# Kernel tuning notes

Measured on AMD Instinct MI355X. Metric: run time of the kernel, lower is better.

## Reference

```python
import jax, jax.numpy as jnp
import numpy as np

LANES = 4
EPS = 1e-8

def _rms_norm(z):
    # utils.rms: RMS-normalize along last dim
    return z * jax.lax.rsqrt(jnp.mean(z * z, axis=-1, keepdims=True) + EPS)

def _combine(left, right, W):
    # one scan combine step: tiny SDPA over the 4 lanes per token
    B, T, C = left.shape
    hd = C // LANES
    q = left.reshape(B, T, LANES, hd)
    k = right.reshape(B, T, LANES, hd)
    # ProcrustesButterflyLinear: orthogonal mixing of the two operands
    v = ((left + right) @ W).reshape(B, T, LANES, hd)
    scores = jnp.einsum('btld,btmd->btlm', q, k) * (hd ** -0.5)  # [B,T,4,4]
    att = jax.nn.softmax(scores, axis=-1)
    z = jnp.einsum('btlm,btmd->btld', att, v)
    denom = (1.0 + jnp.arange(LANES, dtype=z.dtype))[None, None, :, None]
    z = _rms_norm(z) / denom
    return left + z.reshape(B, T, C)

def _pscan2(x, W, identity):
    # parallel inclusive scan (Hillis-Steele, log2(T) combine steps)
    B, T, C = x.shape
    d = 1
    while d < T:
        ident = jnp.broadcast_to(identity.astype(x.dtype), (B, d, C))
        shifted = jnp.concatenate([ident, x[:, :-d]], axis=1)
        x = _combine(shifted, x, W)
        d *= 2
    return x

def setup_inputs() -> dict:
    key = jax.random.key(0)
    ks = jax.random.split(key, 6)
    B, T, C = 4, 2048, 1024
    s = 0.02
    x = jax.random.normal(ks[0], (B, T, C), dtype=jnp.float32)
    W_up = jax.random.normal(ks[1], (C, C), dtype=jnp.float32) * s
    W_v = jax.random.normal(ks[2], (C, C), dtype=jnp.float32) * s
    W_proj = jax.random.normal(ks[3], (C, C), dtype=jnp.float32) * s
    identity = jax.random.uniform(ks[4], (C,), dtype=jnp.float32)
    W_scan_raw = jax.random.normal(ks[5], (C, C), dtype=jnp.float32) * s
    return {"x": x, "W_up": W_up, "W_v": W_v, "W_proj": W_proj,
            "identity": identity, "W_scan_raw": W_scan_raw}

def reference(x, W_up, W_v, W_proj, identity, W_scan_raw):
    # Procrustes orthogonalization of the scanner weight (nearest orthogonal matrix)
    U, _, Vt = jnp.linalg.svd(W_scan_raw, full_matrices=False)
    W = U @ Vt
    q = x @ W_up.T      # self.up(x)
    v = x @ W_v.T       # self.v_attn(x)
    q = _pscan2(q, W, identity)
    Y = (q * v) @ W_proj.T   # c_proj; dropout = identity at eval
    return (Y, q)
```

## Files before the change

### kernel.cpp

```cpp
#include <hip/hip_runtime.h>
#include <hip/hip_bf16.h>

#define DEVINL __device__ __forceinline__

constexpr int B_   = 4;
constexpr int T_   = 2048;
constexpr int C_   = 1024;
constexpr int NTOK = B_ * T_;
constexpr int HD   = 256;

typedef unsigned short u16;
typedef __attribute__((ext_vector_type(8))) short  frag_ab;
typedef __attribute__((ext_vector_type(4))) float  frag_cd;
typedef __attribute__((ext_vector_type(8))) u16    u16x8;
typedef __attribute__((ext_vector_type(4))) u16    u16x4;

DEVINL float bf2f(u16 u) {
    unsigned int x = ((unsigned int)u) << 16;
    return __uint_as_float(x);
}
DEVINL u16 f2bf(float f) {
    unsigned int x = __float_as_uint(f);
    unsigned int r = (x + 0x7fffu + ((x >> 16) & 1u)) >> 16;
    return (u16)r;
}
DEVINL void split2(float f, u16& h, u16& l) {
    h = f2bf(f);
    l = f2bf(f - bf2f(h));
}
DEVINL float wave_reduce(float v) {
    #pragma unroll
    for (int off = 32; off > 0; off >>= 1) v += __shfl_down(v, off, 64);
    return v;
}
DEVINL void gl_lds16(const void* g, void* l) {
    __builtin_amdgcn_global_load_lds(
        (const __attribute__((address_space(1))) unsigned int*)g,
        (__attribute__((address_space(3))) unsigned int*)l, 16, 0, 0);
}

DEVINL void swizzle_block(int& bx, int& by) {
    const int hw = (int)(blockIdx.x + gridDim.x * blockIdx.y);
    if (gridDim.x == 8 && gridDim.y == 64) {
        const int xcd = hw & 7, idx = hw >> 3;
        by = xcd * 8 + (idx & 7);
        bx = idx >> 3;
    } else { bx = blockIdx.x; by = blockIdx.y; }
}

__global__ __launch_bounds__(256) void detect_k(const u16* __restrict__ w,
                                                int* __restrict__ flag)
{
    int tid = threadIdx.x;
    int cnt = 0;
    for (int i = tid; i < 4096; i += 256) {
        u16 u = w[2 * i];
        int e = (u >> 7) & 0xFF;
        if (u == 0 || (e >= 96 && e <= 134)) cnt++;
    }
    __shared__ int sh[256];
    sh[tid] = cnt; __syncthreads();
    for (int s = 128; s > 0; s >>= 1) {
        if (tid < s) sh[tid] += sh[tid + s];
        __syncthreads();
    }
    if (tid == 0) *flag = (sh[0] > 2048) ? 1 : 0;
}

__global__ __launch_bounds__(256) void conv_k(const void* __restrict__ src,
                                              float* __restrict__ dst, int n,
                                              const int* __restrict__ flag)
{
    int i = blockIdx.x * 256 + threadIdx.x;
    if (i >= n) return;
    if (*flag) dst[i] = bf2f(((const u16*)src)[i]);
    else       dst[i] = ((const float*)src)[i];
}

__global__ __launch_bounds__(256) void conv_split_k(const void* __restrict__ src,
                                                    u16* __restrict__ H,
                                                    u16* __restrict__ L, int n4,
                                                    const int* __restrict__ flag)
{
    int i = blockIdx.x * 256 + threadIdx.x;
    if (i >= n4) return;
    float f[4];
    if (*flag) {
        u16x4 u = ((const u16x4*)src)[i];
        f[0] = bf2f(u[0]); f[1] = bf2f(u[1]); f[2] = bf2f(u[2]); f[3] = bf2f(u[3]);
    } else {
        float4 v = ((const float4*)src)[i];
        f[0] = v.x; f[1] = v.y; f[2] = v.z; f[3] = v.w;
    }
    u16x4 h, lo;
    #pragma unroll
    for (int r = 0; r < 4; ++r) { u16 a, b; split2(f[r], a, b); h[r] = a; lo[r] = b; }
    ((u16x4*)H)[i] = h; ((u16x4*)L)[i] = lo;
}

__global__ __launch_bounds__(256) void convb_k(const void* __restrict__ src,
                                               u16* __restrict__ out, int n4,
                                               const int* __restrict__ flag)
{
    int i = blockIdx.x * 256 + threadIdx.x;
    if (i >= n4) return;
    u16x4 o;
    if (*flag) {
        o = ((const u16x4*)src)[i];
    } else {
        float4 v = ((const float4*)src)[i];
        o[0] = f2bf(v.x); o[1] = f2bf(v.y); o[2] = f2bf(v.z); o[3] = f2bf(v.w);
    }
    ((u16x4*)out)[i] = o;
}

__global__ __launch_bounds__(256) void sumsq_k(const float* __restrict__ X,
                                               float* __restrict__ sumsq)
{
    int i = blockIdx.x * 256 + threadIdx.x;
    float f = X[i];
    float p = wave_reduce(f * f);
    __shared__ float r[4];
    int lane = threadIdx.x & 63, w = threadIdx.x >> 6;
    if (lane == 0) r[w] = p;
    __syncthreads();
    if (threadIdx.x == 0) atomicAdd(sumsq, r[0] + r[1] + r[2] + r[3]);
}

__global__ __launch_bounds__(256) void scale_k(float* __restrict__ X,
                                               const float* __restrict__ sumsq)
{
    int i = blockIdx.x * 256 + threadIdx.x;
    float F = sqrtf(*sumsq);
    float s = 16.0f / (1.1f * F);
    X[i] *= s;
}

__global__ __launch_bounds__(256) void split_k(const float* __restrict__ X,
                                               u16* __restrict__ H,
                                               u16* __restrict__ L, int n)
{
    int i = blockIdx.x * 256 + threadIdx.x;
    if (i >= n) return;
    u16 hi, lo; split2(X[i], hi, lo);
    H[i] = hi; L[i] = lo;
}

__global__ __launch_bounds__(256) void transpose_split_k(
    const float* __restrict__ W, u16* __restrict__ Th, u16* __restrict__ Tl)
{
    __shared__ float tile[32][33];
    const int k0 = blockIdx.y * 32;
    const int n0 = blockIdx.x * 32;
    const int tx = threadIdx.x & 31, ty = threadIdx.x >> 5;
    #pragma unroll
    for (int r = 0; r < 32; r += 8)
        tile[ty + r][tx] = W[(size_t)(k0 + ty + r) * C_ + n0 + tx];
    __syncthreads();
    #pragma unroll
    for (int r = 0; r < 32; r += 8) {
        float f = tile[tx][ty + r];
        size_t idx = (size_t)(n0 + ty + r) * C_ + k0 + tx;
        u16 hi, lo; split2(f, hi, lo);
        Th[idx] = hi; Tl[idx] = lo;
    }
}

__global__ __launch_bounds__(256) void gemm_split64(
    const u16* __restrict__ Ah, const u16* __restrict__ Al,
    const u16* __restrict__ Bh, const u16* __restrict__ Bl,
    float* __restrict__ Cf, u16* __restrict__ Ch, u16* __restrict__ Cl,
    const float* __restrict__ D, float alpha, float beta,
    int M, int N, int K,
    u16* __restrict__ Th, u16* __restrict__ Tl)
{
    __shared__ u16 sAh[2][4][64][32];
    __shared__ u16 sAl[2][4][64][32];
    __shared__ u16 sBh[2][4][64][32];
    __shared__ u16 sBl[2][4][64][32];

    const int bm = blockIdx.y * 64, bn = blockIdx.x * 64;
    const int tid = threadIdx.x;
    const int l = tid & 63, w = tid >> 6;
    const int mbase = (w & 1) * 32, nbase = (w >> 1) * 32;
    const int lrow = l & 15, kq = (l >> 4) << 3;

    frag_cd acc[2][2];
    #pragma unroll
    for (int i = 0; i < 2; ++i)
        #pragma unroll
        for (int j = 0; j < 2; ++j)
            #pragma unroll
            for (int r = 0; r < 4; ++r) acc[i][j][r] = 0.0f;

    auto STAGE = [&](int buf, int k0) {
        #pragma unroll
        for (int half = 0; half < 4; ++half) {
            const int c   = tid + half * 256;
            const int ks  = c >> 8;
            const int row = (c >> 2) & 63;
            const int ko  = ks * 32 + (c & 3) * 8;
            const size_t ga = (size_t)(bm + row) * K + k0 + ko;
            const size_t gb = (size_t)(bn + row) * K + k0 + ko;
            gl_lds16(Ah + ga, &sAh[0][0][0][0] + buf * 8192 + (c << 3));
            gl_lds16(Al + ga, &sAl[0][0][0][0] + buf * 8192 + (c << 3));
            gl_lds16(Bh + gb, &sBh[0][0][0][0] + buf * 8192 + (c << 3));
            gl_lds16(Bl + gb, &sBl[0][0][0][0] + buf * 8192 + (c << 3));
        }
    };

    STAGE(0, 0);
    __syncthreads();
    const int NT = K >> 7;
    int cur = 0;
    for (int t = 0; t < NT; ++t) {
        if (t + 1 < NT) STAGE(cur ^ 1, (t + 1) << 7);
        #pragma unroll
        for (int ks = 0; ks < 4; ++ks) {
            frag_ab ah[2], al2[2], bh[2], bl2[2];
            #pragma unroll
            for (int i = 0; i < 2; ++i) {
                const int ro = mbase + 16 * i + lrow;
                ah[i]  = *(const frag_ab*)&sAh[cur][ks][ro][kq];
                al2[i] = *(const frag_ab*)&sAl[cur][ks][ro][kq];
            }
            #pragma unroll
            for (int j = 0; j < 2; ++j) {
                const int ro = nbase + 16 * j + lrow;
                bh[j]  = *(const frag_ab*)&sBh[cur][ks][ro][kq];
                bl2[j] = *(const frag_ab*)&sBl[cur][ks][ro][kq];
            }
            #pragma unroll
            for (int i = 0; i < 2; ++i)
                #pragma unroll
                for (int j = 0; j < 2; ++j) {
                    acc[i][j] = __builtin_amdgcn_mfma_f32_16x16x32_bf16(
                        ah[i], bh[j], acc[i][j], 0, 0, 0);
                    acc[i][j] = __builtin_amdgcn_mfma_f32_16x16x32_bf16(
                        al2[i], bh[j], acc[i][j], 0, 0, 0);
                    acc[i][j] = __builtin_amdgcn_mfma_f32_16x16x32_bf16(
                        ah[i], bl2[j], acc[i][j], 0, 0, 0);
                    acc[i][j] = __builtin_amdgcn_mfma_f32_16x16x32_bf16(
                        al2[i], bl2[j], acc[i][j], 0, 0, 0);
                }
        }
        __syncthreads();
        cur ^= 1;
    }

    const int quad = l >> 4;
    u16* tileH = &sAh[0][0][0][0];
    u16* tileL = &sAl[0][0][0][0];
    #pragma unroll
    for (int i = 0; i < 2; ++i) {
        #pragma unroll
        for (int j = 0; j < 2; ++j) {
            const int coln = bn + nbase + 16 * j + lrow;
            #pragma unroll
            for (int r = 0; r < 4; ++r) {
                const int rowm = bm + mbase + 16 * i + quad * 4 + r;
                const size_t idx = (size_t)rowm * N + coln;
                float v = beta * acc[i][j][r];
                if (D) v += alpha * D[idx];
                if (Cf) Cf[idx] = v;
                u16 hi, lo; split2(v, hi, lo);
                if (Ch) { Ch[idx] = hi; Cl[idx] = lo; }
                if (Th) {
                    const int rl = mbase + 16 * i + quad * 4 + r;
                    const int cl = nbase + 16 * j + lrow;
                    tileH[rl * 68 + cl] = hi;
                    tileL[rl * 68 + cl] = lo;
                }
            }
        }
    }
    if (Th) {
        __syncthreads();
        const int jj  = tid >> 2;
        const int ii0 = (tid & 3) << 4;
        u16x8 ph0, ph1, pl0, pl1;
        #pragma unroll
        for (int e = 0; e < 8; ++e) {
            ph0[e] = tileH[(ii0 + e) * 68 + jj];
            pl0[e] = tileL[(ii0 + e) * 68 + jj];
            ph1[e] = tileH[(ii0 + 8 + e) * 68 + jj];
            pl1[e] = tileL[(ii0 + 8 + e) * 68 + jj];
        }
        const size_t tb = (size_t)(bn + jj) * N + bm + ii0;
        *(u16x8*)&Th[tb]     = ph0;
        *(u16x8*)&Th[tb + 8] = ph1;
        *(u16x8*)&Tl[tb]     = pl0;
        *(u16x8*)&Tl[tb + 8] = pl1;
    }
}

__global__ __launch_bounds__(256) void gemm_split(
    const u16* __restrict__ Ah, const u16* __restrict__ Al,
    const u16* __restrict__ Bh, const u16* __restrict__ Bl,
    float* __restrict__ Cf, u16* __restrict__ Ch, u16* __restrict__ Cl,
    int M, int N, int K)
{
    __shared__ u16 sAh[2][128][32];
    __shared__ u16 sAl[2][128][32];
    __shared__ u16 sBh[2][128][32];
    __shared__ u16 sBl[2][128][32];

    int bx, by; swizzle_block(bx, by);
    const int bm = by * 128, bn = bx * 128;
    const int tid = threadIdx.x;
    const int l = tid & 63, w = tid >> 6;
    const int mbase = (w & 1) * 64, nbase = (w >> 1) * 64;
    const int lrow = l & 15, kq = (l >> 4) << 3;

    frag_cd acc[4][4];
    #pragma unroll
    for (int i = 0; i < 4; ++i)
        #pragma unroll
        for (int j = 0; j < 4; ++j)
            #pragma unroll
            for (int r = 0; r < 4; ++r) acc[i][j][r] = 0.0f;

    auto STAGE = [&](int buf, int k0) {
        #pragma unroll
        for (int half = 0; half < 2; ++half) {
            const int c   = tid + half * 256;
            const int row = c >> 2;
            const int ko  = (c & 3) << 3;
            const size_t ga = (size_t)(bm + row) * K + k0 + ko;
            const size_t gb = (size_t)(bn + row) * K + k0 + ko;
            gl_lds16(Ah + ga, &sAh[buf][0][0] + (c << 3));
            gl_lds16(Al + ga, &sAl[buf][0][0] + (c << 3));
            gl_lds16(Bh + gb, &sBh[buf][0][0] + (c << 3));
            gl_lds16(Bl + gb, &sBl[buf][0][0] + (c << 3));
        }
    };

    STAGE(0, 0);
    __syncthreads();
    const int NT = K >> 5;
    int cur = 0;
    for (int t = 0; t < NT; ++t) {
        if (t + 1 < NT) STAGE(cur ^ 1, (t + 1) << 5);
        frag_ab ah[4], al4[4], bh[4], bl4[4];
        #pragma unroll
        for (int i = 0; i < 4; ++i) {
            const int ro = mbase + 16 * i + lrow;
            ah[i]  = *(const frag_ab*)&sAh[cur][ro][kq];
            al4[i] = *(const frag_ab*)&sAl[cur][ro][kq];
        }
        #pragma unroll
        for (int j = 0; j < 4; ++j) {
            const int ro = nbase + 16 * j + lrow;
            bh[j]  = *(const frag_ab*)&sBh[cur][ro][kq];
            bl4[j] = *(const frag_ab*)&sBl[cur][ro][kq];
        }
        #pragma unroll
        for (int i = 0; i < 4; ++i)
            #pragma unroll
            for (int j = 0; j < 4; ++j) {
                acc[i][j] = __builtin_amdgcn_mfma_f32_16x16x32_bf16(
                    ah[i], bh[j], acc[i][j], 0, 0, 0);
                acc[i][j] = __builtin_amdgcn_mfma_f32_16x16x32_bf16(
                    al4[i], bh[j], acc[i][j], 0, 0, 0);
                acc[i][j] = __builtin_amdgcn_mfma_f32_16x16x32_bf16(
                    ah[i], bl4[j], acc[i][j], 0, 0, 0);
            }
        __syncthreads();
        cur ^= 1;
    }

    const int quad = l >> 4;
    #pragma unroll
    for (int i = 0; i < 4; ++i) {
        #pragma unroll
        for (int j = 0; j < 4; ++j) {
            const int coln = bn + nbase + 16 * j + lrow;
            #pragma unroll
            for (int r = 0; r < 4; ++r) {
                const int rowm = bm + mbase + 16 * i + quad * 4 + r;
                const size_t idx = (size_t)rowm * N + coln;
                float v = acc[i][j][r];
                if (Cf) Cf[idx] = v;
                if (Ch) { u16 hi, lo; split2(v, hi, lo); Ch[idx] = hi; Cl[idx] = lo; }
            }
        }
    }
}

__global__ __launch_bounds__(256) void gemm_bf16(
    const u16* __restrict__ Ab, const u16* __restrict__ Bb,
    void* __restrict__ Cdst, int cmode, const int* __restrict__ flag,
    int M, int N, int K)
{
    __shared__ u16 As[2][2][128][32];
    __shared__ u16 Bs[2][2][128][32];
    const int cbf = (cmode == 1) ? *flag : 0;

    int bx, by; swizzle_block(bx, by);
    const int bm = by * 128, bn = bx * 128;
    const int tid = threadIdx.x;
    const int l = tid & 63, w = tid >> 6;
    const int mbase = (w & 1) * 64, nbase = (w >> 1) * 64;
    const int lrow = l & 15, kq = (l >> 4) << 3;

    frag_cd acc[4][4];
    #pragma unroll
    for (int i = 0; i < 4; ++i)
        #pragma unroll
        for (int j = 0; j < 4; ++j)
            #pragma unroll
            for (int r = 0; r < 4; ++r) acc[i][j][r] = 0.0f;

    auto STAGE = [&](int buf, int k0) {
        #pragma unroll
        for (int half = 0; half < 4; ++half) {
            const int c   = tid + half * 256;
            const int ks  = c >> 9;
            const int row = (c >> 2) & 127;
            const int ko  = ks * 32 + (c & 3) * 8;
            const size_t ga = (size_t)(bm + row) * K + k0 + ko;
            const size_t gb = (size_t)(bn + row) * K + k0 + ko;
            gl_lds16(Ab + ga, &As[buf][0][0][0] + (c << 3));
            gl_lds16(Bb + gb, &Bs[buf][0][0][0] + (c << 3));
        }
    };

    STAGE(0, 0);
    __syncthreads();
    const int NT = K >> 6;
    int cur = 0;
    for (int t = 0; t < NT; ++t) {
        if (t + 1 < NT) STAGE(cur ^ 1, (t + 1) << 6);
        #pragma unroll
        for (int ks = 0; ks < 2; ++ks) {
            frag_ab a[4], b[4];
            #pragma unroll
            for (int i = 0; i < 4; ++i)
                a[i] = *(const frag_ab*)&As[cur][ks][mbase + 16 * i + lrow][kq];
            #pragma unroll
            for (int j = 0; j < 4; ++j)
                b[j] = *(const frag_ab*)&Bs[cur][ks][nbase + 16 * j + lrow][kq];
            #pragma unroll
            for (int i = 0; i < 4; ++i)
                #pragma unroll
                for (int j = 0; j < 4; ++j)
                    acc[i][j] = __builtin_amdgcn_mfma_f32_16x16x32_bf16(
                        a[i], b[j], acc[i][j], 0, 0, 0);
        }
        __syncthreads();
        cur ^= 1;
    }

    const int quad = l >> 4;
    #pragma unroll
    for (int i = 0; i < 4; ++i) {
        #pragma unroll
        for (int j = 0; j < 4; ++j) {
            const int coln = bn + nbase + 16 * j + lrow;
            #pragma unroll
            for (int r = 0; r < 4; ++r) {
                const int rowm = bm + mbase + 16 * i + quad * 4 + r;
                const size_t idx = (size_t)rowm * N + coln;
                float v = acc[i][j][r];
                if (cbf) ((u16*)Cdst)[idx] = f2bf(v);
                else     ((float*)Cdst)[idx] = v;
            }
        }
    }
}

__global__ __launch_bounds__(256) void qvb_k(const u16* __restrict__ qh,
                                             const u16* __restrict__ ql,
                                             const float* __restrict__ V,
                                             u16* __restrict__ out, int n4)
{
    int i = blockIdx.x * 256 + threadIdx.x;
    if (i >= n4) return;
    u16x4 h = ((const u16x4*)qh)[i], lo = ((const u16x4*)ql)[i];
    float4 v = ((const float4*)V)[i];
    u16x4 o;
    o[0] = f2bf((bf2f(h[0]) + bf2f(lo[0])) * v.x);
    o[1] = f2bf((bf2f(h[1]) + bf2f(lo[1])) * v.y);
    o[2] = f2bf((bf2f(h[2]) + bf2f(lo[2])) * v.z);
    o[3] = f2bf((bf2f(h[3]) + bf2f(lo[3])) * v.w);
    ((u16x4*)out)[i] = o;
}

__global__ __launch_bounds__(256) void store_split_k(
    const u16* __restrict__ h, const u16* __restrict__ l,
    void* __restrict__ out, int n4, size_t off4,
    const int* __restrict__ flag)
{
    int i = blockIdx.x * 256 + threadIdx.x;
    if (i >= n4) return;
    u16x4 hh = ((const u16x4*)h)[i], ll = ((const u16x4*)l)[i];
    float4 f;
    f.x = bf2f(hh[0]) + bf2f(ll[0]);
    f.y = bf2f(hh[1]) + bf2f(ll[1]);
    f.z = bf2f(hh[2]) + bf2f(ll[2]);
    f.w = bf2f(hh[3]) + bf2f(ll[3]);
    if (*flag) {
        u16x4 o; o[0] = f2bf(f.x); o[1] = f2bf(f.y); o[2] = f2bf(f.z); o[3] = f2bf(f.w);
        ((u16x4*)out)[off4 + i] = o;
    } else {
        ((float4*)out)[off4 + i] = f;
    }
}

__global__ __launch_bounds__(256) void idw2_k(
    const float* __restrict__ identf, const float* __restrict__ W,
    float* __restrict__ idW)
{
    const int b = blockIdx.x;
    const int j = threadIdx.x;
    float a0 = 0, a1 = 0, a2 = 0, a3 = 0;
    #pragma unroll
    for (int ii = 0; ii < 16; ++ii) {
        const int i = b * 16 + ii;
        const float s = identf[i];
        const float* row = W + (size_t)i * C_;
        a0 += s * row[j];
        a1 += s * row[j + 256];
        a2 += s * row[j + 512];
        a3 += s * row[j + 768];
    }
    atomicAdd(idW + j, a0);       atomicAdd(idW + j + 256, a1);
    atomicAdd(idW + j + 512, a2); atomicAdd(idW + j + 768, a3);
}

__global__ __launch_bounds__(256) void combine3_k(
    const u16* __restrict__ curh, const u16* __restrict__ curl,
    const float* __restrict__ xW,
    const float* __restrict__ idW, const float* __restrict__ identf,
    u16* __restrict__ nxth, u16* __restrict__ nxtl, int d)
{
    const int token = blockIdx.x;
    const int t = token & (T_ - 1);
    const int tid = threadIdx.x;
    const bool hl = (t >= d);
    const size_t rbase = (size_t)token * C_;
    const size_t lbase = hl ? (size_t)(token - d) * C_ : 0;
    const float* leftW  = hl ? xW + lbase : idW;
    const float* rightW = xW + rbase;

    const int e0   = tid << 2;
    const int a    = tid >> 6;
    const int dd   = (tid & 63) << 2;
    const int lane = tid & 63;

    float q4[4], k4[4], v4[4];
    {
        u16x4 kh = *(const u16x4*)&curh[rbase + e0];
        u16x4 kl = *(const u16x4*)&curl[rbase + e0];
        #pragma unroll
        for (int e = 0; e < 4; ++e) k4[e] = bf2f(kh[e]) + bf2f(kl[e]);
        if (hl) {
            u16x4 qh = *(const u16x4*)&curh[lbase + e0];
            u16x4 ql = *(const u16x4*)&curl[lbase + e0];
            #pragma unroll
            for (int e = 0; e < 4; ++e) q4[e] = bf2f(qh[e]) + bf2f(ql[e]);
        } else {
            float4 iv = *(const float4*)&identf[e0];
            q4[0] = iv.x; q4[1] = iv.y; q4[2] = iv.z; q4[3] = iv.w;
        }
        float4 lw = *(const float4*)&leftW[e0];
        float4 rw = *(const float4*)&rightW[e0];
        v4[0] = lw.x + rw.x; v4[1] = lw.y + rw.y;
        v4[2] = lw.z + rw.z; v4[3] = lw.w + rw.w;
    }

    __shared__ float ks[4][256];
    __shared__ float vs[4][256];
    __shared__ float red[16];
    __shared__ float att[16];
    __shared__ float rs4[4];
    {
        float4 kv = { k4[0], k4[1], k4[2], k4[3] };
        float4 vv = { v4[0], v4[1], v4[2], v4[3] };
        *(float4*)&ks[a][dd] = kv;
        *(float4*)&vs[a][dd] = vv;
    }
    __syncthreads();

    #pragma unroll
    for (int b = 0; b < 4; ++b) {
        float4 kk = *(const float4*)&ks[b][dd];
        float pp = q4[0] * kk.x + q4[1] * kk.y + q4[2] * kk.z + q4[3] * kk.w;
        float sb = wave_reduce(pp);
        if (lane == 0) red[a * 4 + b] = sb * 0.0625f;
    }
    __syncthreads();
    if (tid < 4) {
        float s0 = red[tid * 4 + 0], s1 = red[tid * 4 + 1];
        float s2 = red[tid * 4 + 2], s3 = red[tid * 4 + 3];
        float mx = fmaxf(fmaxf(s0, s1), fmaxf(s2, s3));
        float x0 = __expf(s0 - mx), x1 = __expf(s1 - mx);
        float x2 = __expf(s2 - mx), x3 = __expf(s3 - mx);
        float inv = 1.0f / (x0 + x1 + x2 + x3);
        att[tid * 4 + 0] = x0 * inv; att[tid * 4 + 1] = x1 * inv;
        att[tid * 4 + 2] = x2 * inv; att[tid * 4 + 3] = x3 * inv;
    }
    __syncthreads();

    const float a0 = att[a * 4 + 0], a1 = att[a * 4 + 1];
    const float a2 = att[a * 4 + 2], a3 = att[a * 4 + 3];
    float4 v0 = *(const float4*)&vs[0][dd];
    float4 v1 = *(const float4*)&vs[1][dd];
    float4 v2 = *(const float4*)&vs[2][dd];
    float4 v3 = *(const float4*)&vs[3][dd];
    float z4[4];
    z4[0] = a0 * v0.x + a1 * v1.x + a2 * v2.x + a3 * v3.x;
    z4[1] = a0 * v0.y + a1 * v1.y + a2 * v2.y + a3 * v3.y;
    z4[2] = a0 * v0.z + a1 * v1.z + a2 * v2.z + a3 * v3.z;
    z4[3] = a0 * v0.w + a1 * v1.w + a2 * v2.w + a3 * v3.w;

    float ssp = z4[0] * z4[0] + z4[1] * z4[1] + z4[2] * z4[2] + z4[3] * z4[3];
    float ss = wave_reduce(ssp);
    if (lane == 0) rs4[a] = rsqrtf(ss * (1.0f / HD) + 1e-8f);
    __syncthreads();

    const float rs = rs4[a] * (1.0f / (float)(a + 1));
    u16x4 oh, ol;
    #pragma unroll
    for (int e = 0; e < 4; ++e) {
        float out = q4[e] + z4[e] * rs;
        u16 hi, lo; split2(out, hi, lo);
        oh[e] = hi; ol[e] = lo;
    }
    *(u16x4*)&nxth[rbase + e0] = oh;
    *(u16x4*)&nxtl[rbase + e0] = ol;
}

extern "C" void kernel_launch(void* const* d_in, const int* in_sizes, int n_in,
                              void* d_out, int out_size, void* d_ws, size_t ws_size,
                              hipStream_t stream)
{
    const void* x     = d_in[0];
    const void* Wup   = d_in[1];
    const void* Wv    = d_in[2];
    const void* Wproj = d_in[3];
    const void* ident = d_in[4];
    const void* Wraw  = d_in[5];

    float* ws = (float*)d_ws;
    int*   flagp  = (int*)ws;
    float* sumsqp = ws + 1;
    float* W0     = ws + 256;
    float* W1     = W0 + (1 << 20);
    float* identf = W1 + (1 << 20);
    float* idW    = identf + 1024;
    float* F1     = idW + 1024;
    u16*   WTh    = (u16*)(F1 + (size_t)NTOK * C_);
    u16*   WTl    = WTh + (1 << 20);
    u16*   WUh    = WTl + (1 << 20);
    u16*   WUl    = WUh + (1 << 20);
    u16*   Q0h    = WUl + (1 << 20);
    u16*   Q0l    = Q0h + (size_t)NTOK * C_;
    u16*   Q1h    = Q0l + (size_t)NTOK * C_;
    u16*   Q1l    = Q1h + (size_t)NTOK * C_;

    const int NC = C_ * C_;
    const int NX = NTOK * C_;

    detect_k<<<1, 256, 0, stream>>>((const u16*)Wup, flagp);

    hipMemsetAsync(sumsqp, 0, sizeof(float), stream);
    conv_k<<<NC / 256, 256, 0, stream>>>(Wraw, W0, NC, flagp);
    sumsq_k<<<NC / 256, 256, 0, stream>>>(W0, sumsqp);
    scale_k<<<NC / 256, 256, 0, stream>>>(W0, sumsqp);

    u16* Gh   = WUh;  u16* Gl = WUl;
    u16* Xh2[2] = { Q0h,                 Q0h + 2 * (1 << 20) };
    u16* Xl2[2] = { Q0h + (1 << 20),     Q0h + 3 * (1 << 20) };

    split_k<<<NC / 256, 256, 0, stream>>>(W0, Xh2[0], Xl2[0], NC);
    transpose_split_k<<<dim3(32, 32), 256, 0, stream>>>(W0, WTh, WTl);

    float* Xf = W0; float* Yf = W1; int cur = 0;
    const dim3 gNS(16, 16);
    for (int it = 0; it < 23; ++it) {
        bool polish = (it >= 18);
        float a = polish ? 1.5f : 2.0f;
        float b = polish ? -0.5f : -1.0f;
        gemm_split64<<<gNS, 256, 0, stream>>>(WTh, WTl, WTh, WTl,
                                              nullptr, Gh, Gl,
                                              nullptr, 0.0f, 1.0f, C_, C_, C_,
                                              nullptr, nullptr);
        gemm_split64<<<gNS, 256, 0, stream>>>(Xh2[cur], Xl2[cur], Gh, Gl,
                                              Yf, Xh2[cur ^ 1], Xl2[cur ^ 1],
                                              Xf, a, b, C_, C_, C_,
                                              WTh, WTl);
        float* tmp = Xf; Xf = Yf; Yf = tmp; cur ^= 1;
    }

    conv_k<<<4, 256, 0, stream>>>(ident, identf, 1024, flagp);
    hipMemsetAsync(idW, 0, C_ * sizeof(float), stream);
    idw2_k<<<64, 256, 0, stream>>>(identf, Xf, idW);

    const dim3 g128(C_ / 128, NTOK / 128);

    conv_split_k<<<NX / 1024, 256, 0, stream>>>(x, Q1h, Q1l, NX / 4, flagp);
    conv_split_k<<<NC / 1024, 256, 0, stream>>>(Wup, WUh, WUl, NC / 4, flagp);
    gemm_split<<<g128, 256, 0, stream>>>(Q1h, Q1l, WUh, WUl,
                                         nullptr, Q0h, Q0l, NTOK, C_, C_);

    u16 *ch = Q0h, *cl = Q0l, *nh = Q1h, *nl = Q1l;
    for (int d = 1; d < T_; d <<= 1) {
        gemm_split<<<g128, 256, 0, stream>>>(ch, cl, WTh, WTl,
                                             F1, nullptr, nullptr, NTOK, C_, C_);
        combine3_k<<<NTOK, 256, 0, stream>>>(ch, cl, F1, idW, identf, nh, nl, d);
        u16* t1 = ch; ch = nh; nh = t1;
        u16* t2 = cl; cl = nl; nl = t2;
    }

    convb_k<<<NC / 1024, 256, 0, stream>>>(Wv,    WUh, NC / 4, flagp);
    convb_k<<<NC / 1024, 256, 0, stream>>>(Wproj, WUl, NC / 4, flagp);
    convb_k<<<NX / 1024, 256, 0, stream>>>(x,     Q0h, NX / 4, flagp);

    gemm_bf16<<<g128, 256, 0, stream>>>(Q0h, WUh, F1, 0, flagp, NTOK, C_, C_);

    qvb_k<<<NX / 1024, 256, 0, stream>>>(ch, cl, F1, Q0l, NX / 4);
    gemm_bf16<<<g128, 256, 0, stream>>>(Q0l, WUl, d_out, 1, flagp, NTOK, C_, C_);

    store_split_k<<<NX / 1024, 256, 0, stream>>>(ch, cl, d_out, NX / 4,
                                                 (size_t)(NX / 4), flagp);
}
```

Measured before the change: 2.027 ms.

## Use quintic Newton-Schulz for polar factor and fuse small prep kernels

Replaces the 23-step cubic Newton-Schulz orthogonalization (46 GEMMs) with 10 quintic steps (30 GEMMs) plus 5 cubic polish steps (10 GEMMs). The quintic update is folded into GEMM epilogues through an extra scaled addend. Several elementwise conversion, split and store kernels are merged into fewer launches. The scan combine kernel now computes softmax and RMS per wave, without the extra shared-memory barriers. The quintic coefficients converge less tightly, so orthogonality accuracy could suffer if the polish steps are not enough.

```diff
diff --git a/kernel.cpp b/kernel.cpp
--- a/kernel.cpp
+++ b/kernel.cpp
@@ -67,58 +67,14 @@
     if (tid == 0) *flag = (sh[0] > 2048) ? 1 : 0;
 }
 
-__global__ __launch_bounds__(256) void conv_k(const void* __restrict__ src,
-                                              float* __restrict__ dst, int n,
-                                              const int* __restrict__ flag)
+__global__ __launch_bounds__(256) void conv_sumsq_k(const void* __restrict__ src,
+                                                    float* __restrict__ dst,
+                                                    const int* __restrict__ flag,
+                                                    float* __restrict__ sumsq)
 {
     int i = blockIdx.x * 256 + threadIdx.x;
-    if (i >= n) return;
-    if (*flag) dst[i] = bf2f(((const u16*)src)[i]);
-    else       dst[i] = ((const float*)src)[i];
-}
-
-__global__ __launch_bounds__(256) void conv_split_k(const void* __restrict__ src,
-                                                    u16* __restrict__ H,
-                                                    u16* __restrict__ L, int n4,
-                                                    const int* __restrict__ flag)
-{
-    int i = blockIdx.x * 256 + threadIdx.x;
-    if (i >= n4) return;
-    float f[4];
-    if (*flag) {
-        u16x4 u = ((const u16x4*)src)[i];
-        f[0] = bf2f(u[0]); f[1] = bf2f(u[1]); f[2] = bf2f(u[2]); f[3] = bf2f(u[3]);
-    } else {
-        float4 v = ((const float4*)src)[i];
-        f[0] = v.x; f[1] = v.y; f[2] = v.z; f[3] = v.w;
-    }
-    u16x4 h, lo;
-    #pragma unroll
-    for (int r = 0; r < 4; ++r) { u16 a, b; split2(f[r], a, b); h[r] = a; lo[r] = b; }
-    ((u16x4*)H)[i] = h; ((u16x4*)L)[i] = lo;
-}
-
-__global__ __launch_bounds__(256) void convb_k(const void* __restrict__ src,
-                                               u16* __restrict__ out, int n4,
-                                               const int* __restrict__ flag)
-{
-    int i = blockIdx.x * 256 + threadIdx.x;
-    if (i >= n4) return;
-    u16x4 o;
-    if (*flag) {
-        o = ((const u16x4*)src)[i];
-    } else {
-        float4 v = ((const float4*)src)[i];
-        o[0] = f2bf(v.x); o[1] = f2bf(v.y); o[2] = f2bf(v.z); o[3] = f2bf(v.w);
-    }
-    ((u16x4*)out)[i] = o;
-}
-
-__global__ __launch_bounds__(256) void sumsq_k(const float* __restrict__ X,
-                                               float* __restrict__ sumsq)
-{
-    int i = blockIdx.x * 256 + threadIdx.x;
-    float f = X[i];
+    float f = (*flag) ? bf2f(((const u16*)src)[i]) : ((const float*)src)[i];
+    dst[i] = f;
     float p = wave_reduce(f * f);
     __shared__ float r[4];
     int lane = threadIdx.x & 63, w = threadIdx.x >> 6;
@@ -127,23 +83,28 @@
     if (threadIdx.x == 0) atomicAdd(sumsq, r[0] + r[1] + r[2] + r[3]);
 }
 
-__global__ __launch_bounds__(256) void scale_k(float* __restrict__ X,
-                                               const float* __restrict__ sumsq)
+__global__ __launch_bounds__(256) void scale_split_k(float* __restrict__ X,
+                                                     const float* __restrict__ sumsq,
+                                                     u16* __restrict__ H,
+                                                     u16* __restrict__ L)
 {
     int i = blockIdx.x * 256 + threadIdx.x;
     float F = sqrtf(*sumsq);
     float s = 16.0f / (1.1f * F);
-    X[i] *= s;
-}
-
-__global__ __launch_bounds__(256) void split_k(const float* __restrict__ X,
-                                               u16* __restrict__ H,
-                                               u16* __restrict__ L, int n)
-{
-    int i = blockIdx.x * 256 + threadIdx.x;
-    if (i >= n) return;
-    u16 hi, lo; split2(X[i], hi, lo);
+    float f = X[i] * s;
+    X[i] = f;
+    u16 hi, lo; split2(f, hi, lo);
     H[i] = hi; L[i] = lo;
+}
+
+__global__ __launch_bounds__(256) void ident_init_k(const void* __restrict__ ident,
+                                                    float* __restrict__ identf,
+                                                    float* __restrict__ idW,
+                                                    const int* __restrict__ flag)
+{
+    int j = blockIdx.x * 256 + threadIdx.x;
+    identf[j] = (*flag) ? bf2f(((const u16*)ident)[j]) : ((const float*)ident)[j];
+    idW[j] = 0.0f;
 }
 
 __global__ __launch_bounds__(256) void transpose_split_k(
@@ -170,7 +131,8 @@
     const u16* __restrict__ Ah, const u16* __restrict__ Al,
     const u16* __restrict__ Bh, const u16* __restrict__ Bl,
     float* __restrict__ Cf, u16* __restrict__ Ch, u16* __restrict__ Cl,
-    const float* __restrict__ D, float alpha, float beta,
+    const float* __restrict__ D, float alpha,
+    const float* __restrict__ D2, float alpha2, float beta,
     int M, int N, int K,
     u16* __restrict__ Th, u16* __restrict__ Tl)
 {
@@ -261,7 +223,8 @@
                 const int rowm = bm + mbase + 16 * i + quad * 4 + r;
                 const size_t idx = (size_t)rowm * N + coln;
                 float v = beta * acc[i][j][r];
-                if (D) v += alpha * D[idx];
+                if (D)  v += alpha  * D[idx];
+                if (D2) v += alpha2 * D2[idx];
                 if (Cf) Cf[idx] = v;
                 u16 hi, lo; split2(v, hi, lo);
                 if (Ch) { Ch[idx] = hi; Cl[idx] = lo; }
@@ -469,40 +432,76 @@
     }
 }
 
-__global__ __launch_bounds__(256) void qvb_k(const u16* __restrict__ qh,
-                                             const u16* __restrict__ ql,
-                                             const float* __restrict__ V,
-                                             u16* __restrict__ out, int n4)
+__global__ __launch_bounds__(256) void prep_q0_k(
+    const void* __restrict__ x, const void* __restrict__ wup,
+    u16* __restrict__ Xh, u16* __restrict__ Xl,
+    u16* __restrict__ Wh, u16* __restrict__ Wl,
+    const int* __restrict__ flag)
 {
     int i = blockIdx.x * 256 + threadIdx.x;
-    if (i >= n4) return;
+    const int n4x = (NTOK * C_) / 4;
+    const void* src; u16 *H, *L; int idx;
+    if (i < n4x) { src = x;   H = Xh; L = Xl; idx = i; }
+    else         { src = wup; H = Wh; L = Wl; idx = i - n4x; }
+    float f[4];
+    if (*flag) {
+        u16x4 u = ((const u16x4*)src)[idx];
+        f[0] = bf2f(u[0]); f[1] = bf2f(u[1]); f[2] = bf2f(u[2]); f[3] = bf2f(u[3]);
+    } else {
+        float4 v = ((const float4*)src)[idx];
+        f[0] = v.x; f[1] = v.y; f[2] = v.z; f[3] = v.w;
+    }
+    u16x4 h, lo;
+    #pragma unroll
+    for (int r = 0; r < 4; ++r) { u16 a, b; split2(f[r], a, b); h[r] = a; lo[r] = b; }
+    ((u16x4*)H)[idx] = h; ((u16x4*)L)[idx] = lo;
+}
+
+__global__ __launch_bounds__(256) void prep_vy_k(
+    const void* __restrict__ x, const void* __restrict__ wv,
+    const void* __restrict__ wp,
+    u16* __restrict__ xb, u16* __restrict__ wvb, u16* __restrict__ wpb,
+    const int* __restrict__ flag)
+{
+    int i = blockIdx.x * 256 + threadIdx.x;
+    const int n4x = (NTOK * C_) / 4;
+    const int n4c = (C_ * C_) / 4;
+    const void* src; u16* out; int idx;
+    if (i < n4x)            { src = x;  out = xb;  idx = i; }
+    else if (i < n4x + n4c) { src = wv; out = wvb; idx = i - n4x; }
+    else                    { src = wp; out = wpb; idx = i - n4x - n4c; }
+    u16x4 o;
+    if (*flag) {
+        o = ((const u16x4*)src)[idx];
+    } else {
+        float4 v = ((const float4*)src)[idx];
+        o[0] = f2bf(v.x); o[1] = f2bf(v.y); o[2] = f2bf(v.z); o[3] = f2bf(v.w);
+    }
+    ((u16x4*)out)[idx] = o;
+}
+
+__global__ __launch_bounds__(256) void qv_store_k(
+    const u16* __restrict__ qh, const u16* __restrict__ ql,
+    const float* __restrict__ V, u16* __restrict__ qvout,
+    void* __restrict__ out, const int* __restrict__ flag)
+{
+    int i = blockIdx.x * 256 + threadIdx.x;
     u16x4 h = ((const u16x4*)qh)[i], lo = ((const u16x4*)ql)[i];
     float4 v = ((const float4*)V)[i];
+    float r0 = bf2f(h[0]) + bf2f(lo[0]);
+    float r1 = bf2f(h[1]) + bf2f(lo[1]);
+    float r2 = bf2f(h[2]) + bf2f(lo[2]);
+    float r3 = bf2f(h[3]) + bf2f(lo[3]);
     u16x4 o;
-    o[0] = f2bf((bf2f(h[0]) + bf2f(lo[0])) * v.x);
-    o[1] = f2bf((bf2f(h[1]) + bf2f(lo[1])) * v.y);
-    o[2] = f2bf((bf2f(h[2]) + bf2f(lo[2])) * v.z);
-    o[3] = f2bf((bf2f(h[3]) + bf2f(lo[3])) * v.w);
-    ((u16x4*)out)[i] = o;
-}
-
-__global__ __launch_bounds__(256) void store_split_k(
-    const u16* __restrict__ h, const u16* __restrict__ l,
-    void* __restrict__ out, int n4, size_t off4,
-    const int* __restrict__ flag)
-{
-    int i = blockIdx.x * 256 + threadIdx.x;
-    if (i >= n4) return;
-    u16x4 hh = ((const u16x4*)h)[i], ll = ((const u16x4*)l)[i];
-    float4 f;
-    f.x = bf2f(hh[0]) + bf2f(ll[0]);
-    f.y = bf2f(hh[1]) + bf2f(ll[1]);
-    f.z = bf2f(hh[2]) + bf2f(ll[2]);
-    f.w = bf2f(hh[3]) + bf2f(ll[3]);
+    o[0] = f2bf(r0 * v.x); o[1] = f2bf(r1 * v.y);
+    o[2] = f2bf(r2 * v.z); o[3] = f2bf(r3 * v.w);
+    ((u16x4*)qvout)[i] = o;
+    const size_t off4 = (size_t)(NTOK * C_) / 4;
     if (*flag) {
-        u16x4 o; o[0] = f2bf(f.x); o[1] = f2bf(f.y); o[2] = f2bf(f.z); o[3] = f2bf(f.w);
-        ((u16x4*)out)[off4 + i] = o;
+        u16x4 q; q[0] = f2bf(r0); q[1] = f2bf(r1); q[2] = f2bf(r2); q[3] = f2bf(r3);
+        ((u16x4*)out)[off4 + i] = q;
     } else {
+        float4 f; f.x = r0; f.y = r1; f.z = r2; f.w = r3;
         ((float4*)out)[off4 + i] = f;
     }
 }
@@ -528,7 +527,7 @@
     atomicAdd(idW + j + 512, a2); atomicAdd(idW + j + 768, a3);
 }
 
-__global__ __launch_bounds__(256) void combine3_k(
+__global__ __launch_bounds__(256) void combine4_k(
     const u16* __restrict__ curh, const u16* __restrict__ curl,
     const float* __restrict__ xW,
     const float* __restrict__ idW, const float* __restrict__ identf,
@@ -572,8 +571,6 @@
     __shared__ float ks[4][256];
     __shared__ float vs[4][256];
     __shared__ float red[16];
-    __shared__ float att[16];
-    __shared__ float rs4[4];
     {
         float4 kv = { k4[0], k4[1], k4[2], k4[3] };
         float4 vv = { v4[0], v4[1], v4[2], v4[3] };
@@ -590,20 +587,15 @@
         if (lane == 0) red[a * 4 + b] = sb * 0.0625f;
     }
     __syncthreads();
-    if (tid < 4) {
-        float s0 = red[tid * 4 + 0], s1 = red[tid * 4 + 1];
-        float s2 = red[tid * 4 + 2], s3 = red[tid * 4 + 3];
-        float mx = fmaxf(fmaxf(s0, s1), fmaxf(s2, s3));
-        float x0 = __expf(s0 - mx), x1 = __expf(s1 - mx);
-        float x2 = __expf(s2 - mx), x3 = __expf(s3 - mx);
-        float inv = 1.0f / (x0 + x1 + x2 + x3);
-        att[tid * 4 + 0] = x0 * inv; att[tid * 4 + 1] = x1 * inv;
-        att[tid * 4 + 2] = x2 * inv; att[tid * 4 + 3] = x3 * inv;
-    }
-    __syncthreads();
-
-    const float a0 = att[a * 4 + 0], a1 = att[a * 4 + 1];
-    const float a2 = att[a * 4 + 2], a3 = att[a * 4 + 3];
+
+    float s0 = red[a * 4 + 0], s1 = red[a * 4 + 1];
+    float s2 = red[a * 4 + 2], s3 = red[a * 4 + 3];
+    float mx = fmaxf(fmaxf(s0, s1), fmaxf(s2, s3));
+    float x0 = __expf(s0 - mx), x1 = __expf(s1 - mx);
+    float x2 = __expf(s2 - mx), x3 = __expf(s3 - mx);
+    float inv = 1.0f / (x0 + x1 + x2 + x3);
+    const float a0 = x0 * inv, a1 = x1 * inv, a2 = x2 * inv, a3 = x3 * inv;
+
     float4 v0 = *(const float4*)&vs[0][dd];
     float4 v1 = *(const float4*)&vs[1][dd];
     float4 v2 = *(const float4*)&vs[2][dd];
@@ -616,10 +608,9 @@
 
     float ssp = z4[0] * z4[0] + z4[1] * z4[1] + z4[2] * z4[2] + z4[3] * z4[3];
     float ss = wave_reduce(ssp);
-    if (lane == 0) rs4[a] = rsqrtf(ss * (1.0f / HD) + 1e-8f);
-    __syncthreads();
-
-    const float rs = rs4[a] * (1.0f / (float)(a + 1));
+    ss = __shfl(ss, 0, 64);
+    const float rs = rsqrtf(ss * (1.0f / HD) + 1e-8f) * (1.0f / (float)(a + 1));
+
     u16x4 oh, ol;
     #pragma unroll
     for (int e = 0; e < 4; ++e) {
@@ -665,42 +656,55 @@
     detect_k<<<1, 256, 0, stream>>>((const u16*)Wup, flagp);
 
     hipMemsetAsync(sumsqp, 0, sizeof(float), stream);
-    conv_k<<<NC / 256, 256, 0, stream>>>(Wraw, W0, NC, flagp);
-    sumsq_k<<<NC / 256, 256, 0, stream>>>(W0, sumsqp);
-    scale_k<<<NC / 256, 256, 0, stream>>>(W0, sumsqp);
-
-    u16* Gh   = WUh;  u16* Gl = WUl;
-    u16* Xh2[2] = { Q0h,                 Q0h + 2 * (1 << 20) };
-    u16* Xl2[2] = { Q0h + (1 << 20),     Q0h + 3 * (1 << 20) };
-
-    split_k<<<NC / 256, 256, 0, stream>>>(W0, Xh2[0], Xl2[0], NC);
+    conv_sumsq_k<<<NC / 256, 256, 0, stream>>>(Wraw, W0, flagp, sumsqp);
+
+    u16* Gh = WUh;  u16* Gl = WUl;
+    u16* Xh2[2] = { Q0h,             Q0h + 2 * (1 << 20) };
+    u16* Xl2[2] = { Q0h + (1 << 20), Q0h + 3 * (1 << 20) };
+    u16* Hh = Q0h + 4 * (1 << 20);
+    u16* Hl = Q0h + 5 * (1 << 20);
+    float* Hf = F1;
+
+    scale_split_k<<<NC / 256, 256, 0, stream>>>(W0, sumsqp, Xh2[0], Xl2[0]);
     transpose_split_k<<<dim3(32, 32), 256, 0, stream>>>(W0, WTh, WTl);
 
     float* Xf = W0; float* Yf = W1; int cur = 0;
     const dim3 gNS(16, 16);
-    for (int it = 0; it < 23; ++it) {
-        bool polish = (it >= 18);
-        float a = polish ? 1.5f : 2.0f;
-        float b = polish ? -0.5f : -1.0f;
+    const float aQ = 3.4445f, bQ = -4.7750f, cQ = 2.0315f;
+    for (int it = 0; it < 10; ++it) {
         gemm_split64<<<gNS, 256, 0, stream>>>(WTh, WTl, WTh, WTl,
                                               nullptr, Gh, Gl,
-                                              nullptr, 0.0f, 1.0f, C_, C_, C_,
-                                              nullptr, nullptr);
+                                              nullptr, 0.0f, nullptr, 0.0f, 1.0f,
+                                              C_, C_, C_, nullptr, nullptr);
+        gemm_split64<<<gNS, 256, 0, stream>>>(Xh2[cur], Xl2[cur], Gh, Gl,
+                                              Hf, Hh, Hl,
+                                              nullptr, 0.0f, nullptr, 0.0f, 1.0f,
+                                              C_, C_, C_, nullptr, nullptr);
+        gemm_split64<<<gNS, 256, 0, stream>>>(Hh, Hl, Gh, Gl,
+                                              Yf, Xh2[cur ^ 1], Xl2[cur ^ 1],
+                                              Xf, aQ, Hf, bQ, cQ,
+                                              C_, C_, C_, WTh, WTl);
+        float* tmp = Xf; Xf = Yf; Yf = tmp; cur ^= 1;
+    }
+    for (int it = 0; it < 5; ++it) {
+        gemm_split64<<<gNS, 256, 0, stream>>>(WTh, WTl, WTh, WTl,
+                                              nullptr, Gh, Gl,
+                                              nullptr, 0.0f, nullptr, 0.0f, 1.0f,
+                                              C_, C_, C_, nullptr, nullptr);
         gemm_split64<<<gNS, 256, 0, stream>>>(Xh2[cur], Xl2[cur], Gh, Gl,
                                               Yf, Xh2[cur ^ 1], Xl2[cur ^ 1],
-                                              Xf, a, b, C_, C_, C_,
-                                              WTh, WTl);
+                                              Xf, 1.5f, nullptr, 0.0f, -0.5f,
+                                              C_, C_, C_, WTh, WTl);
         float* tmp = Xf; Xf = Yf; Yf = tmp; cur ^= 1;
     }
 
-    conv_k<<<4, 256, 0, stream>>>(ident, identf, 1024, flagp);
-    hipMemsetAsync(idW, 0, C_ * sizeof(float), stream);
+    ident_init_k<<<4, 256, 0, stream>>>(ident, identf, idW, flagp);
     idw2_k<<<64, 256, 0, stream>>>(identf, Xf, idW);
 
     const dim3 g128(C_ / 128, NTOK / 128);
 
-    conv_split_k<<<NX / 1024, 256, 0, stream>>>(x, Q1h, Q1l, NX / 4, flagp);
-    conv_split_k<<<NC / 1024, 256, 0, stream>>>(Wup, WUh, WUl, NC / 4, flagp);
+    prep_q0_k<<<(NX + NC) / 1024, 256, 0, stream>>>(x, Wup, Q1h, Q1l,
+                                                    WUh, WUl, flagp);
     gemm_split<<<g128, 256, 0, stream>>>(Q1h, Q1l, WUh, WUl,
                                          nullptr, Q0h, Q0l, NTOK, C_, C_);
 
@@ -708,20 +712,17 @@
     for (int d = 1; d < T_; d <<= 1) {
         gemm_split<<<g128, 256, 0, stream>>>(ch, cl, WTh, WTl,
                                              F1, nullptr, nullptr, NTOK, C_, C_);
-        combine3_k<<<NTOK, 256, 0, stream>>>(ch, cl, F1, idW, identf, nh, nl, d);
+        combine4_k<<<NTOK, 256, 0, stream>>>(ch, cl, F1, idW, identf, nh, nl, d);
         u16* t1 = ch; ch = nh; nh = t1;
         u16* t2 = cl; cl = nl; nl = t2;
     }
 
-    convb_k<<<NC / 1024, 256, 0, stream>>>(Wv,    WUh, NC / 4, flagp);
-    convb_k<<<NC / 1024, 256, 0, stream>>>(Wproj, WUl, NC / 4, flagp);
-    convb_k<<<NX / 1024, 256, 0, stream>>>(x,     Q0h, NX / 4, flagp);
+    prep_vy_k<<<(NX + 2 * NC) / 1024, 256, 0, stream>>>(x, Wv, Wproj,
+                                                        Q0h, WUh, WUl, flagp);
 
     gemm_bf16<<<g128, 256, 0, stream>>>(Q0h, WUh, F1, 0, flagp, NTOK, C_, C_);
 
-    qvb_k<<<NX / 1024, 256, 0, stream>>>(ch, cl, F1, Q0l, NX / 4);
+    qv_store_k<<<NX / 1024, 256, 0, stream>>>(ch, cl, F1, Q0l, d_out, flagp);
+
     gemm_bf16<<<g128, 256, 0, stream>>>(Q0l, WUl, d_out, 1, flagp, NTOK, C_, C_);
-
-    store_split_k<<<NX / 1024, 256, 0, stream>>>(ch, cl, d_out, NX / 4,
-                                                 (size_t)(NX / 4), flagp);
-}
+}
```

Result: faster. 1.891 ms (-6.7%).
